# Kernel tuning notes

Hardware: AMD Instinct MI355X
Metric: run time of the kernel (lower is better)

The kernel has to match this reference:

```python
import jax, jax.numpy as jnp
import numpy as np

H = 256
LOG_STD_MIN, LOG_STD_MAX = -20.0, 2.0


def setup_inputs() -> dict:
    key = jax.random.key(0)
    ks = jax.random.split(key, 12)
    B, T, F, A = 256, 1000, 64, 16
    s_in = 1.0 / np.sqrt(H)
    inp = {
        "observations": jax.random.normal(ks[0], (B, T, F), jnp.float32),
        # LSTM params (PyTorch gate order: i, f, g, o)
        "W_ih": jax.random.uniform(ks[1], (4 * H, F), jnp.float32, -s_in, s_in),
        "W_hh": jax.random.uniform(ks[2], (4 * H, H), jnp.float32, -s_in, s_in),
        "b_ih": jax.random.uniform(ks[3], (4 * H,), jnp.float32, -s_in, s_in),
        "b_hh": jax.random.uniform(ks[4], (4 * H,), jnp.float32, -s_in, s_in),
        # layer2: Linear(256 -> 256)
        "W2": jax.random.uniform(ks[5], (H, H), jnp.float32, -s_in, s_in),
        "b2": jax.random.uniform(ks[6], (H,), jnp.float32, -s_in, s_in),
        # means head: Linear(256 -> A)
        "Wm": jax.random.uniform(ks[7], (A, H), jnp.float32, -s_in, s_in),
        "bm": jax.random.uniform(ks[8], (A,), jnp.float32, -s_in, s_in),
        # log_stds head: Linear(256 -> A)
        "Ws": jax.random.uniform(ks[9], (A, H), jnp.float32, -s_in, s_in),
        "bs": jax.random.uniform(ks[10], (A,), jnp.float32, -s_in, s_in),
    }
    return inp


def _lstm(observations, W_ih, W_hh, b_ih, b_hh):
    B, T, F = observations.shape
    # Precompute the input-to-gate projection for all timesteps: [T, B, 4H]
    xg = jnp.einsum("btf,gf->tbg", observations, W_ih) + (b_ih + b_hh)
    W_hh_T = W_hh.T  # [H, 4H]

    def step(carry, xg_t):
        h, c = carry  # [B, H] each
        gates = xg_t + h @ W_hh_T  # [B, 4H]
        i, f, g, o = jnp.split(gates, 4, axis=-1)
        i = jax.nn.sigmoid(i)
        f = jax.nn.sigmoid(f)
        g = jnp.tanh(g)
        o = jax.nn.sigmoid(o)
        c = f * c + i * g
        h = o * jnp.tanh(c)
        return (h, c), h

    h0 = jnp.zeros((B, H), observations.dtype)
    c0 = jnp.zeros((B, H), observations.dtype)
    _, hs = jax.lax.scan(step, (h0, c0), xg)  # hs: [T, B, H]
    return jnp.transpose(hs, (1, 0, 2))  # [B, T, H]


def reference(observations, W_ih, W_hh, b_ih, b_hh, W2, b2, Wm, bm, Ws, bs):
    x = _lstm(observations, W_ih, W_hh, b_ih, b_hh)  # [B, T, H]
    x = jax.nn.relu(jnp.einsum("bth,oh->bto", x, W2) + b2)  # [B, T, H]
    means = jnp.einsum("bth,ah->bta", x, Wm) + bm  # [B, T, A]
    log_stds = jnp.einsum("bth,ah->bta", x, Ws) + bs  # [B, T, A]
    stds = jnp.exp(jnp.clip(log_stds, LOG_STD_MIN, LOG_STD_MAX))
    return (means, stds)
```

## Files before the change

### kernel.cpp

```cpp
#include <hip/hip_runtime.h>


#define NB 256
#define NT 1000
#define NF 64
#define NH 256
#define NG 1024
#define NA 16
#define NTHREADS 512
#define CHUNK 8
#define NCHUNK (NT / CHUNK)

typedef _Float16 h2 __attribute__((ext_vector_type(2)));
typedef _Float16 h8 __attribute__((ext_vector_type(8)));
typedef float f4 __attribute__((ext_vector_type(4)));

__device__ __forceinline__ float fdot2(h2 a, h2 b, float c) {
  return __builtin_amdgcn_fdot2(a, b, c, false);
}
__device__ __forceinline__ float fexp2(float x) { return __builtin_amdgcn_exp2f(x); }
__device__ __forceinline__ float frcp(float x) { return __builtin_amdgcn_rcpf(x); }
__device__ __forceinline__ float sigmoidf_(float x) {
  return frcp(1.f + fexp2(-1.4426950408889634f * x));
}
__device__ __forceinline__ float tanhfast(float x) {
  float a = fabsf(x);
  float e = fexp2(-2.8853900817779268f * a);
  float r = (1.f - e) * frcp(1.f + e);
  return __builtin_copysignf(r, x);
}
__device__ __forceinline__ float dot8(h8 x, h8 w, float acc) {
  acc = fdot2(__builtin_shufflevector(x, x, 0, 1), __builtin_shufflevector(w, w, 0, 1), acc);
  acc = fdot2(__builtin_shufflevector(x, x, 2, 3), __builtin_shufflevector(w, w, 2, 3), acc);
  acc = fdot2(__builtin_shufflevector(x, x, 4, 5), __builtin_shufflevector(w, w, 4, 5), acc);
  acc = fdot2(__builtin_shufflevector(x, x, 6, 7), __builtin_shufflevector(w, w, 6, 7), acc);
  return acc;
}

__global__ void prep_kernel(const float* __restrict__ Wih, const float* __restrict__ Whh,
                            const float* __restrict__ bih, const float* __restrict__ bhh,
                            const float* __restrict__ W2, const float* __restrict__ Wm,
                            const float* __restrict__ Ws,
                            h2* __restrict__ whh, h2* __restrict__ wih,
                            h2* __restrict__ w2w, h2* __restrict__ wmh,
                            float* __restrict__ bg) {
  int i = blockIdx.x * 256 + threadIdx.x;
  if (i < 1024 * 128) {
    int j = i >> 7, p = i & 127;
    whh[i] = h2{(_Float16)Whh[j * 256 + 2 * p], (_Float16)Whh[j * 256 + 2 * p + 1]};
  }
  if (i < 1024 * 32) {
    int j = i >> 5, p = i & 31;
    wih[i] = h2{(_Float16)Wih[j * 64 + 2 * p], (_Float16)Wih[j * 64 + 2 * p + 1]};
  }
  if (i < 256 * 128) {
    int j = i >> 7, p = i & 127;
    w2w[i] = h2{(_Float16)W2[j * 256 + 2 * p], (_Float16)W2[j * 256 + 2 * p + 1]};
  }
  if (i < 32 * 128) {
    int j = i >> 7, p = i & 127;
    float v0, v1;
    if (j < 16) { v0 = Wm[j * 256 + 2 * p]; v1 = Wm[j * 256 + 2 * p + 1]; }
    else        { v0 = Ws[(j - 16) * 256 + 2 * p]; v1 = Ws[(j - 16) * 256 + 2 * p + 1]; }
    wmh[i] = h2{(_Float16)v0, (_Float16)v1};
  }
  if (i < 1024) bg[i] = bih[i] + bhh[i];
}

__global__ __launch_bounds__(NTHREADS, 2) void actor_kernel(
    const float* __restrict__ obs,
    const h2* __restrict__ whh, const h2* __restrict__ wih,
    const h2* __restrict__ w2w, const h2* __restrict__ wmh,
    const float* __restrict__ bg, const float* __restrict__ b2,
    const float* __restrict__ bm, const float* __restrict__ bs,
    float* __restrict__ out) {
  __shared__ __align__(16) h8 whh_l[8 * 1024];
  __shared__ __align__(16) _Float16 xg_l[CHUNK * NG];
  __shared__ __align__(16) f4 pbuf[NH];
  __shared__ __align__(16) h2 hbuf[NH / 2];
  __shared__ __align__(16) h2 hch[CHUNK * NH / 2];
  __shared__ __align__(16) h2 xbuf[CHUNK * NF / 2];
  __shared__ __align__(16) h2 x2b[CHUNK * NH / 2];

  const int tid = threadIdx.x;
  const int b = blockIdx.x;
  const int half = tid >> 8;
  const int j = tid & 255;

  h8 wreg[48];
  {
    const volatile h8* vw = (const volatile h8*)whh;
#pragma unroll
    for (int g = 0; g < 4; g++)
#pragma unroll
      for (int m = 0; m < 12; m++)
        wreg[g * 12 + m] = vw[(g * 256 + j) * 32 + half * 16 + 4 + m];
  }
  {
    const h8* whh8 = (const h8*)whh;
    for (int k = tid; k < 8 * 1024; k += NTHREADS) {
      int q = k >> 10, row = k & 1023;
      whh_l[q * 1024 + row] = whh8[row * 32 + (q >> 2) * 16 + (q & 3)];
    }
  }
  if (tid < NH / 2) hbuf[tid] = h2{(_Float16)0.f, (_Float16)0.f};
  float c_state = 0.f;
  const int r0 = tid, r1 = tid + NTHREADS;
  const float biasg0 = bg[r0], biasg1 = bg[r1];
  const float b2v = b2[tid & 255];
  const int oh = tid & 31;
  const float hbv = (oh < NA) ? bm[oh] : bs[oh - NA];
  __syncthreads();

  const float* obs_b = obs + (size_t)b * NT * NF;
  float* out_means = out;
  float* out_stds = out + (size_t)NB * NT * NA;

  for (int ch = 0; ch < NCHUNK; ++ch) {
    const int t0 = ch * CHUNK;

    if (tid < 128) {
      int t = tid >> 4, fq = tid & 15;
      f4 v = *(const f4*)(obs_b + (size_t)(t0 + t) * NF + fq * 4);
      xbuf[t * 32 + fq * 2] = h2{(_Float16)v[0], (_Float16)v[1]};
      xbuf[t * 32 + fq * 2 + 1] = h2{(_Float16)v[2], (_Float16)v[3]};
    }
    __syncthreads();

#pragma unroll
    for (int rr = 0; rr < 2; ++rr) {
      const int row = rr ? r1 : r0;
      const float bias = rr ? biasg1 : biasg0;
      float acc[CHUNK];
#pragma unroll
      for (int t = 0; t < CHUNK; t++) acc[t] = bias;
      const h8* wrow = (const h8*)wih + row * 8;
#pragma unroll
      for (int jh = 0; jh < 2; jh++) {
        h8 w[4];
#pragma unroll
        for (int q = 0; q < 4; q++) w[q] = wrow[jh * 4 + q];
#pragma unroll
        for (int t = 0; t < CHUNK; t++) {
#pragma unroll
          for (int q = 0; q < 4; q++) {
            h8 xv = *(const h8*)&xbuf[t * 32 + jh * 16 + q * 4];
            acc[t] = dot8(xv, w[q], acc[t]);
          }
        }
      }
#pragma unroll
      for (int t = 0; t < CHUNK; t++) xg_l[t * NG + row] = (_Float16)acc[t];
    }
    __syncthreads();

    for (int t = 0; t < CHUNK; t++) {
      float a0 = 0.f, a1 = 0.f, a2 = 0.f, a3 = 0.f;
#pragma unroll
      for (int p4 = 0; p4 < 4; p4++) {
        h8 hv = *(const h8*)&hbuf[half * 64 + p4 * 4];
        const h8* wl = &whh_l[(half * 4 + p4) * 1024 + j];
        a0 = dot8(hv, wl[0], a0);
        a1 = dot8(hv, wl[256], a1);
        a2 = dot8(hv, wl[512], a2);
        a3 = dot8(hv, wl[768], a3);
      }
#pragma unroll
      for (int m = 0; m < 12; m++) {
        h8 hv = *(const h8*)&hbuf[half * 64 + 16 + 4 * m];
        a0 = dot8(hv, wreg[m], a0);
        a1 = dot8(hv, wreg[12 + m], a1);
        a2 = dot8(hv, wreg[24 + m], a2);
        a3 = dot8(hv, wreg[36 + m], a3);
      }
      if (half) pbuf[j] = f4{a0, a1, a2, a3};
      __syncthreads();
      if (!half) {
        f4 o4 = pbuf[j];
        float gi = a0 + o4.x + (float)xg_l[t * NG + j];
        float gf = a1 + o4.y + (float)xg_l[t * NG + 256 + j];
        float gg = a2 + o4.z + (float)xg_l[t * NG + 512 + j];
        float go = a3 + o4.w + (float)xg_l[t * NG + 768 + j];
        gi = sigmoidf_(gi);
        gf = sigmoidf_(gf);
        gg = tanhfast(gg);
        go = sigmoidf_(go);
        c_state = gf * c_state + gi * gg;
        float hval = go * tanhfast(c_state);
        _Float16 hh = (_Float16)hval;
        ((_Float16*)hbuf)[j] = hh;
        ((_Float16*)hch)[t * NH + j] = hh;
      }
      __syncthreads();
    }

    {
      const int o = tid & 255;
      const int tb = (tid >> 8) * 4;
      float acc[4] = {b2v, b2v, b2v, b2v};
      const h8* wrow = (const h8*)w2w + o * 32;
#pragma unroll 2
      for (int c = 0; c < 8; c++) {
        h8 w[4];
#pragma unroll
        for (int q = 0; q < 4; q++) w[q] = wrow[c * 4 + q];
#pragma unroll
        for (int tt = 0; tt < 4; tt++) {
#pragma unroll
          for (int q = 0; q < 4; q++) {
            h8 xv = *(const h8*)&hch[(tb + tt) * 128 + c * 16 + q * 4];
            acc[tt] = dot8(xv, w[q], acc[tt]);
          }
        }
      }
#pragma unroll
      for (int tt = 0; tt < 4; tt++)
        ((_Float16*)x2b)[(tb + tt) * NH + o] = (_Float16)fmaxf(acc[tt], 0.f);
    }
    __syncthreads();

    if (tid < 256) {
      const int tt = tid >> 5;
      const h8* wrow = (const h8*)wmh + oh * 32;
      float acc = 0.f;
#pragma unroll 4
      for (int c = 0; c < 32; c++) {
        h8 xv = *(const h8*)&x2b[tt * 128 + c * 4];
        acc = dot8(xv, wrow[c], acc);
      }
      acc += hbv;
      const size_t idx = ((size_t)b * NT + (t0 + tt)) * NA + (oh & 15);
      if (oh < NA) {
        out_means[idx] = acc;
      } else {
        float ls = fminf(fmaxf(acc, -20.f), 2.f);
        out_stds[idx] = fexp2(1.4426950408889634f * ls);
      }
    }
  }
}

extern "C" void kernel_launch(void* const* d_in, const int* in_sizes, int n_in,
                              void* d_out, int out_size, void* d_ws, size_t ws_size,
                              hipStream_t stream) {
  const float* obs = (const float*)d_in[0];
  const float* Wih = (const float*)d_in[1];
  const float* Whh = (const float*)d_in[2];
  const float* bih = (const float*)d_in[3];
  const float* bhh = (const float*)d_in[4];
  const float* W2 = (const float*)d_in[5];
  const float* b2 = (const float*)d_in[6];
  const float* Wm = (const float*)d_in[7];
  const float* bm = (const float*)d_in[8];
  const float* Ws = (const float*)d_in[9];
  const float* bs = (const float*)d_in[10];

  char* ws = (char*)d_ws;
  h2* whh = (h2*)(ws + 0);
  h2* wih = (h2*)(ws + 524288);
  h2* w2w = (h2*)(ws + 655360);
  h2* wmh = (h2*)(ws + 786432);
  float* bg = (float*)(ws + 802816);

  prep_kernel<<<512, 256, 0, stream>>>(Wih, Whh, bih, bhh, W2, Wm, Ws,
                                       whh, wih, w2w, wmh, bg);
  actor_kernel<<<NB, NTHREADS, 0, stream>>>(obs, whh, wih, w2w, wmh, bg, b2, bm,
                                            bs, (float*)d_out);
}
```

Measured before the change: 4.455 ms.

## Use one thread per hidden unit with double-buffered h to halve barriers

Drops the block from 512 to 256 threads so each thread computes all four gates of one hidden unit over the full 256-wide h vector. This removes the cross-half partial-sum exchange through shared memory and one of the two barriers per timestep. The h vector is double-buffered so a single barrier per step is enough, and the xg layout is interleaved so each thread reads its four gates in one load. In exchange, per-thread work per step roughly doubles and 96 h8 weight registers are held per thread, which risks register pressure or spills, and occupancy drops to one block per CU.

```diff
diff --git a/kernel.cpp b/kernel.cpp
--- a/kernel.cpp
+++ b/kernel.cpp
@@ -7,11 +7,12 @@
 #define NH 256
 #define NG 1024
 #define NA 16
-#define NTHREADS 512
+#define NTHREADS 256
 #define CHUNK 8
 #define NCHUNK (NT / CHUNK)
 
 typedef _Float16 h2 __attribute__((ext_vector_type(2)));
+typedef _Float16 h4 __attribute__((ext_vector_type(4)));
 typedef _Float16 h8 __attribute__((ext_vector_type(8)));
 typedef float f4 __attribute__((ext_vector_type(4)));
 
@@ -67,7 +68,7 @@
   if (i < 1024) bg[i] = bih[i] + bhh[i];
 }
 
-__global__ __launch_bounds__(NTHREADS, 2) void actor_kernel(
+__global__ __launch_bounds__(NTHREADS, 1) void actor_kernel(
     const float* __restrict__ obs,
     const h2* __restrict__ whh, const h2* __restrict__ wih,
     const h2* __restrict__ w2w, const h2* __restrict__ wmh,
@@ -76,39 +77,38 @@
     float* __restrict__ out) {
   __shared__ __align__(16) h8 whh_l[8 * 1024];
   __shared__ __align__(16) _Float16 xg_l[CHUNK * NG];
-  __shared__ __align__(16) f4 pbuf[NH];
-  __shared__ __align__(16) h2 hbuf[NH / 2];
-  __shared__ __align__(16) h2 hch[CHUNK * NH / 2];
+  __shared__ __align__(16) h8 hbuf[2][NH / 8];
+  __shared__ __align__(16) _Float16 hch[CHUNK * NH];
   __shared__ __align__(16) h2 xbuf[CHUNK * NF / 2];
-  __shared__ __align__(16) h2 x2b[CHUNK * NH / 2];
+  __shared__ __align__(16) _Float16 x2b[CHUNK * NH];
 
   const int tid = threadIdx.x;
   const int b = blockIdx.x;
-  const int half = tid >> 8;
-  const int j = tid & 255;
-
-  h8 wreg[48];
+  const int j = tid;
+
+  h8 wreg[96];
   {
     const volatile h8* vw = (const volatile h8*)whh;
 #pragma unroll
     for (int g = 0; g < 4; g++)
 #pragma unroll
-      for (int m = 0; m < 12; m++)
-        wreg[g * 12 + m] = vw[(g * 256 + j) * 32 + half * 16 + 4 + m];
+      for (int m = 0; m < 24; m++)
+        wreg[g * 24 + m] = vw[(g * 256 + j) * 32 + 8 + m];
   }
   {
     const h8* whh8 = (const h8*)whh;
     for (int k = tid; k < 8 * 1024; k += NTHREADS) {
       int q = k >> 10, row = k & 1023;
-      whh_l[q * 1024 + row] = whh8[row * 32 + (q >> 2) * 16 + (q & 3)];
-    }
-  }
-  if (tid < NH / 2) hbuf[tid] = h2{(_Float16)0.f, (_Float16)0.f};
+      whh_l[q * 1024 + row] = whh8[row * 32 + q];
+    }
+  }
+  if (tid < 32) hbuf[0][tid] = h8{0, 0, 0, 0, 0, 0, 0, 0};
   float c_state = 0.f;
-  const int r0 = tid, r1 = tid + NTHREADS;
-  const float biasg0 = bg[r0], biasg1 = bg[r1];
-  const float b2v = b2[tid & 255];
-  const int oh = tid & 31;
+  float bg4[4];
+#pragma unroll
+  for (int g = 0; g < 4; g++) bg4[g] = bg[g * 256 + j];
+  const float b2v = b2[j];
+  const int oh = j & 31;
   const float hbv = (oh < NA) ? bm[oh] : bs[oh - NA];
   __syncthreads();
 
@@ -128,106 +128,87 @@
     __syncthreads();
 
 #pragma unroll
-    for (int rr = 0; rr < 2; ++rr) {
-      const int row = rr ? r1 : r0;
-      const float bias = rr ? biasg1 : biasg0;
+    for (int g = 0; g < 4; g++) {
+      const h8* wrow = (const h8*)wih + (g * 256 + j) * 8;
+      h8 w[8];
+#pragma unroll
+      for (int q = 0; q < 8; q++) w[q] = wrow[q];
       float acc[CHUNK];
 #pragma unroll
-      for (int t = 0; t < CHUNK; t++) acc[t] = bias;
-      const h8* wrow = (const h8*)wih + row * 8;
-#pragma unroll
-      for (int jh = 0; jh < 2; jh++) {
-        h8 w[4];
-#pragma unroll
-        for (int q = 0; q < 4; q++) w[q] = wrow[jh * 4 + q];
-#pragma unroll
-        for (int t = 0; t < CHUNK; t++) {
-#pragma unroll
-          for (int q = 0; q < 4; q++) {
-            h8 xv = *(const h8*)&xbuf[t * 32 + jh * 16 + q * 4];
-            acc[t] = dot8(xv, w[q], acc[t]);
-          }
-        }
-      }
-#pragma unroll
-      for (int t = 0; t < CHUNK; t++) xg_l[t * NG + row] = (_Float16)acc[t];
+      for (int t = 0; t < CHUNK; t++) acc[t] = bg4[g];
+#pragma unroll
+      for (int t = 0; t < CHUNK; t++)
+#pragma unroll
+        for (int q = 0; q < 8; q++)
+          acc[t] = dot8(*(const h8*)&xbuf[t * 32 + q * 4], w[q], acc[t]);
+#pragma unroll
+      for (int t = 0; t < CHUNK; t++) xg_l[t * NG + j * 4 + g] = (_Float16)acc[t];
     }
     __syncthreads();
 
     for (int t = 0; t < CHUNK; t++) {
+      const int st = t0 + t;
+      const int rb = st & 1;
       float a0 = 0.f, a1 = 0.f, a2 = 0.f, a3 = 0.f;
 #pragma unroll
-      for (int p4 = 0; p4 < 4; p4++) {
-        h8 hv = *(const h8*)&hbuf[half * 64 + p4 * 4];
-        const h8* wl = &whh_l[(half * 4 + p4) * 1024 + j];
+      for (int q = 0; q < 8; q++) {
+        h8 hv = hbuf[rb][q];
+        const h8* wl = &whh_l[q * 1024 + j];
         a0 = dot8(hv, wl[0], a0);
         a1 = dot8(hv, wl[256], a1);
         a2 = dot8(hv, wl[512], a2);
         a3 = dot8(hv, wl[768], a3);
       }
 #pragma unroll
-      for (int m = 0; m < 12; m++) {
-        h8 hv = *(const h8*)&hbuf[half * 64 + 16 + 4 * m];
+      for (int m = 0; m < 24; m++) {
+        h8 hv = hbuf[rb][8 + m];
         a0 = dot8(hv, wreg[m], a0);
-        a1 = dot8(hv, wreg[12 + m], a1);
-        a2 = dot8(hv, wreg[24 + m], a2);
-        a3 = dot8(hv, wreg[36 + m], a3);
-      }
-      if (half) pbuf[j] = f4{a0, a1, a2, a3};
+        a1 = dot8(hv, wreg[24 + m], a1);
+        a2 = dot8(hv, wreg[48 + m], a2);
+        a3 = dot8(hv, wreg[72 + m], a3);
+      }
+      h4 xg4 = *(const h4*)&xg_l[t * NG + j * 4];
+      float gi = sigmoidf_(a0 + (float)xg4[0]);
+      float gf = sigmoidf_(a1 + (float)xg4[1]);
+      float gg = tanhfast(a2 + (float)xg4[2]);
+      float go = sigmoidf_(a3 + (float)xg4[3]);
+      c_state = gf * c_state + gi * gg;
+      float hval = go * tanhfast(c_state);
+      _Float16 hh = (_Float16)hval;
+      ((_Float16*)hbuf[rb ^ 1])[j] = hh;
+      hch[t * NH + j] = hh;
       __syncthreads();
-      if (!half) {
-        f4 o4 = pbuf[j];
-        float gi = a0 + o4.x + (float)xg_l[t * NG + j];
-        float gf = a1 + o4.y + (float)xg_l[t * NG + 256 + j];
-        float gg = a2 + o4.z + (float)xg_l[t * NG + 512 + j];
-        float go = a3 + o4.w + (float)xg_l[t * NG + 768 + j];
-        gi = sigmoidf_(gi);
-        gf = sigmoidf_(gf);
-        gg = tanhfast(gg);
-        go = sigmoidf_(go);
-        c_state = gf * c_state + gi * gg;
-        float hval = go * tanhfast(c_state);
-        _Float16 hh = (_Float16)hval;
-        ((_Float16*)hbuf)[j] = hh;
-        ((_Float16*)hch)[t * NH + j] = hh;
-      }
-      __syncthreads();
     }
 
     {
-      const int o = tid & 255;
-      const int tb = (tid >> 8) * 4;
-      float acc[4] = {b2v, b2v, b2v, b2v};
-      const h8* wrow = (const h8*)w2w + o * 32;
+      float acc[CHUNK];
+#pragma unroll
+      for (int t = 0; t < CHUNK; t++) acc[t] = b2v;
+      const h8* wrow = (const h8*)w2w + j * 32;
 #pragma unroll 2
-      for (int c = 0; c < 8; c++) {
+      for (int c4 = 0; c4 < 8; c4++) {
         h8 w[4];
 #pragma unroll
-        for (int q = 0; q < 4; q++) w[q] = wrow[c * 4 + q];
-#pragma unroll
-        for (int tt = 0; tt < 4; tt++) {
-#pragma unroll
-          for (int q = 0; q < 4; q++) {
-            h8 xv = *(const h8*)&hch[(tb + tt) * 128 + c * 16 + q * 4];
-            acc[tt] = dot8(xv, w[q], acc[tt]);
-          }
-        }
-      }
-#pragma unroll
-      for (int tt = 0; tt < 4; tt++)
-        ((_Float16*)x2b)[(tb + tt) * NH + o] = (_Float16)fmaxf(acc[tt], 0.f);
+        for (int q = 0; q < 4; q++) w[q] = wrow[c4 * 4 + q];
+#pragma unroll
+        for (int t = 0; t < CHUNK; t++)
+#pragma unroll
+          for (int q = 0; q < 4; q++)
+            acc[t] = dot8(*(const h8*)&hch[t * NH + c4 * 32 + q * 8], w[q], acc[t]);
+      }
+#pragma unroll
+      for (int t = 0; t < CHUNK; t++)
+        x2b[t * NH + j] = (_Float16)fmaxf(acc[t], 0.f);
     }
     __syncthreads();
 
-    if (tid < 256) {
-      const int tt = tid >> 5;
+    {
+      const int tt = j >> 5;
       const h8* wrow = (const h8*)wmh + oh * 32;
       float acc = 0.f;
 #pragma unroll 4
-      for (int c = 0; c < 32; c++) {
-        h8 xv = *(const h8*)&x2b[tt * 128 + c * 4];
-        acc = dot8(xv, wrow[c], acc);
-      }
+      for (int c = 0; c < 32; c++)
+        acc = dot8(*(const h8*)&x2b[tt * NH + c * 8], wrow[c], acc);
       acc += hbv;
       const size_t idx = ((size_t)b * NT + (t0 + tt)) * NA + (oh & 15);
       if (oh < NA) {
```

Result: slower. 6.739 ms (+51.3%).
